# Kernel tuning notes

Hardware: AMD Instinct MI355X
Metric: run time of the kernel (lower is better)

The kernel has to match this reference:

```python
import jax, jax.numpy as jnp
import numpy as np

D_MODEL = 512
NUM_HEADS = 8
HEAD_DIM = D_MODEL // NUM_HEADS
BATCH = 4
SEQ = 2048
NEG_INF = -1e9  # large negative instead of -inf so fully-masked rows stay finite


def setup_inputs() -> dict:
    key = jax.random.key(0)
    k1, k2, k3, k4 = jax.random.split(key, 4)
    x = jax.random.normal(k1, (BATCH, SEQ, D_MODEL), dtype=jnp.float32)
    mask = jnp.zeros((1, 1, SEQ, SEQ), dtype=jnp.float32)  # unused: paded_mask path taken
    paded_mask = jax.random.randint(k2, (BATCH, SEQ), 0, 2).astype(bool)
    W_qkv = jax.random.normal(k3, (D_MODEL, 3 * D_MODEL), dtype=jnp.float32) * (D_MODEL ** -0.5)
    W_out = jax.random.normal(k4, (D_MODEL, D_MODEL), dtype=jnp.float32) * (D_MODEL ** -0.5)
    return {"x": x, "mask": mask, "paded_mask": paded_mask, "W_qkv": W_qkv, "W_out": W_out}


def reference(x, mask, paded_mask, W_qkv, W_out):
    B, S, D = x.shape
    H, hd = NUM_HEADS, HEAD_DIM
    qkv = x @ W_qkv                                   # [B,S,3D]
    # Faithful to original: reshape (NOT transpose) (B,S,H,3hd) -> (B,H,S,3hd)
    qkv = qkv.reshape(B, S, H, 3 * hd).reshape(B, H, S, 3 * hd)
    q, k, v = jnp.split(qkv, 3, axis=3)               # each [B,H,S,hd]
    scaled = jnp.einsum("bhqd,bhkd->bhqk", q, k) / (hd ** 0.5)
    valid = paded_mask.astype(scaled.dtype)           # [B,S]
    # masked_padding_Decoder: softmax over valid keys for valid query rows,
    # zeros on invalid rows and invalid columns.
    logits = jnp.where(paded_mask[:, None, None, :], scaled, NEG_INF)
    att = jax.nn.softmax(logits, axis=-1)
    att = att * valid[:, None, :, None] * valid[:, None, None, :]
    values = jnp.einsum("bhqk,bhkd->bhqd", att, v)    # [B,H,S,hd]
    # Faithful to original: plain reshape (B,H,S,hd) -> (B,S,D)
    values = values.reshape(B, S, H * hd)
    return values @ W_out
```

## Files before the change

kernel.cpp:

```cpp
#include <hip/hip_runtime.h>
#include <hip/hip_bf16.h>
#include <math.h>
#include <stdint.h>

#define BATCH   4
#define SEQ     2048
#define DMODEL  512
#define NHEADS  8
#define HDIM    64
#define QKV_N   (3*DMODEL)

typedef short bf8  __attribute__((ext_vector_type(8)));
typedef float f32x4 __attribute__((ext_vector_type(4)));

#define MFMA16(a,b,c) __builtin_amdgcn_mfma_f32_16x16x32_bf16((a),(b),(c),0,0,0)

__device__ inline unsigned short f2bf(float f){
  unsigned int u = __float_as_uint(f);
  u += 0x7FFFu + ((u >> 16) & 1u);
  return (unsigned short)(u >> 16);
}

__device__ inline unsigned int pack_bf2(float a, float b){
  __hip_bfloat162 h = __float22bfloat162_rn(make_float2(a, b));
  return *reinterpret_cast<unsigned int*>(&h);
}

__device__ __forceinline__ float exp2_hw(float x){
#if defined(__has_builtin)
#if __has_builtin(__builtin_amdgcn_exp2f)
  return __builtin_amdgcn_exp2f(x);
#else
  float r; asm("v_exp_f32 %0, %1" : "=v"(r) : "v"(x)); return r;
#endif
#else
  float r; asm("v_exp_f32 %0, %1" : "=v"(r) : "v"(x)); return r;
#endif
}

__device__ __forceinline__ void gload_lds16(const unsigned short* g,
                                            unsigned short* l){
  __builtin_amdgcn_global_load_lds(
      (const __attribute__((address_space(1))) unsigned int*)g,
      (__attribute__((address_space(3))) unsigned int*)l,
      16, 0, 0);
}

__global__ __launch_bounds__(256) void prep(
    const float* __restrict__ x, const float* __restrict__ Wqkv,
    const float* __restrict__ Wout, unsigned short* __restrict__ Xh,
    unsigned short* __restrict__ WqkvT, unsigned short* __restrict__ WoutT)
{
  __shared__ unsigned short Ts[64][72];
  const int t = threadIdx.x;
  const int bx = blockIdx.x;
  if (bx < 2048) {
    const int i = bx*256 + t;
    const float4 a = reinterpret_cast<const float4*>(x)[2*i];
    const float4 b = reinterpret_cast<const float4*>(x)[2*i+1];
    uint4 o; unsigned short* us = reinterpret_cast<unsigned short*>(&o);
    us[0]=f2bf(a.x); us[1]=f2bf(a.y); us[2]=f2bf(a.z); us[3]=f2bf(a.w);
    us[4]=f2bf(b.x); us[5]=f2bf(b.y); us[6]=f2bf(b.z); us[7]=f2bf(b.w);
    reinterpret_cast<uint4*>(Xh)[i] = o;
    return;
  }
  const float* in; unsigned short* out; int R, C, gx, gy;
  if (bx < 2048 + 192) {
    const int bid = bx - 2048;
    gx = bid % 24; gy = bid / 24; in = Wqkv; out = WqkvT; R = DMODEL; C = QKV_N;
  } else {
    const int bid = bx - 2240;
    gx = bid % 8;  gy = bid / 8;  in = Wout; out = WoutT; R = DMODEL; C = DMODEL;
  }
  const int r0 = gy<<6, c0 = gx<<6;
  const int rr = t>>2, cs = (t&3)<<4;
#pragma unroll
  for (int p=0;p<4;++p){
    float4 v = *reinterpret_cast<const float4*>(in + (size_t)(r0+rr)*C + c0 + cs + p*4);
    Ts[rr][cs+p*4+0]=f2bf(v.x); Ts[rr][cs+p*4+1]=f2bf(v.y);
    Ts[rr][cs+p*4+2]=f2bf(v.z); Ts[rr][cs+p*4+3]=f2bf(v.w);
  }
  __syncthreads();
  const int cc = t>>2, rs = (t&3)<<4;
#pragma unroll
  for (int p=0;p<4;++p){
    ushort4 o;
    o.x = Ts[rs+p*4+0][cc]; o.y = Ts[rs+p*4+1][cc];
    o.z = Ts[rs+p*4+2][cc]; o.w = Ts[rs+p*4+3][cc];
    *reinterpret_cast<ushort4*>(out + (size_t)(c0+cc)*R + r0 + rs + p*4) = o;
  }
}

__global__ __launch_bounds__(256) void gemm_qkv_mfma(
    const unsigned short* __restrict__ A, const unsigned short* __restrict__ Bt,
    unsigned short* __restrict__ QKV)
{
  __shared__ unsigned short As[128][64];
  __shared__ unsigned short Bs[128][64];
  const int t = threadIdx.x;
  const int w = t>>6, lane = t&63, quad = lane>>4, l15 = lane&15;
  const int wr = (w>>1)<<6, wc = (w&1)<<6;
  const int linear = blockIdx.y*12 + blockIdx.x;
  const int swz = (linear & 7)*96 + (linear >> 3);
  const int m0 = (swz/12)<<7, n0 = (swz%12)<<7;
  const int row = t>>3, seg = t&7;
  const unsigned short* Agp = A  + (size_t)(m0+row)*DMODEL + seg*8;
  const unsigned short* Bgp = Bt + (size_t)(n0+row)*DMODEL + seg*8;
  f32x4 acc[4][4];
#pragma unroll
  for (int i=0;i<4;++i)
#pragma unroll
    for (int j=0;j<4;++j) acc[i][j] = (f32x4){0.f,0.f,0.f,0.f};

  for (int k0=0;k0<DMODEL;k0+=64){
    __syncthreads();
#pragma unroll
    for (int p=0;p<4;++p){
      gload_lds16(Agp + (size_t)p*32*DMODEL + k0, &As[(w<<3)+(p<<5)][0]);
      gload_lds16(Bgp + (size_t)p*32*DMODEL + k0, &Bs[(w<<3)+(p<<5)][0]);
    }
    __syncthreads();
#pragma unroll
    for (int ks=0;ks<2;++ks){
      bf8 af[4], bfr[4];
#pragma unroll
      for (int mi=0;mi<4;++mi)
        af[mi]  = *reinterpret_cast<const bf8*>(&As[wr+mi*16+l15][ks*32+quad*8]);
#pragma unroll
      for (int nj=0;nj<4;++nj)
        bfr[nj] = *reinterpret_cast<const bf8*>(&Bs[wc+(l15<<2)+nj][ks*32+quad*8]);
#pragma unroll
      for (int mi=0;mi<4;++mi)
#pragma unroll
        for (int nj=0;nj<4;++nj) acc[mi][nj] = MFMA16(af[mi], bfr[nj], acc[mi][nj]);
    }
  }
  const int cbase = n0 + wc + (l15<<2);
  bool isq[4];
#pragma unroll
  for (int nj=0;nj<4;++nj) isq[nj] = ((cbase+nj) % 192) < 64;
#pragma unroll
  for (int mi=0;mi<4;++mi)
#pragma unroll
    for (int i=0;i<4;++i){
      const int m = m0 + wr + mi*16 + quad*4 + i;
      unsigned long long pk = 0;
#pragma unroll
      for (int nj=0;nj<4;++nj){
        float v = acc[mi][nj][i];
        if (isq[nj]) v *= 0.18033688f;
        pk |= (unsigned long long)f2bf(v) << (16*nj);
      }
      *reinterpret_cast<unsigned long long*>(QKV + (size_t)m*QKV_N + cbase) = pk;
    }
}

__global__ __launch_bounds__(256) void v_transpose(
    const unsigned short* __restrict__ QKV, unsigned short* __restrict__ VT)
{
  __shared__ unsigned short Td[64][76];
  const int t = threadIdx.x;
  const int bh = blockIdx.y, b = bh>>3, hp = bh&7;
  const int s0 = blockIdx.x<<6;
  const size_t rbase = (size_t)(b*SEQ + hp*256);
  const int sr = t>>2, db = (t&3)<<4;
  const int kk = s0 + sr;
  const unsigned short* vp =
      QKV + (rbase + (kk>>3))*QKV_N + (kk&7)*192 + 128 + db;
  uint4 a = *reinterpret_cast<const uint4*>(vp);
  uint4 c = *reinterpret_cast<const uint4*>(vp + 8);
  const unsigned short* ua = reinterpret_cast<const unsigned short*>(&a);
  const unsigned short* uc = reinterpret_cast<const unsigned short*>(&c);
#pragma unroll
  for (int j=0;j<8;++j) Td[db+j][sr]   = ua[j];
#pragma unroll
  for (int j=0;j<8;++j) Td[db+8+j][sr] = uc[j];
  __syncthreads();
  const int L = t&15, d0 = t>>4;
  unsigned short* Op = VT + (size_t)bh*HDIM*SEQ + s0 + (L<<2);
#pragma unroll
  for (int cc=0;cc<4;++cc){
    const int d = d0 + (cc<<4);
    *reinterpret_cast<unsigned long long*>(Op + (size_t)d*SEQ) =
        *reinterpret_cast<const unsigned long long*>(&Td[d][L<<2]);
  }
}

__global__ __launch_bounds__(512, 4) void attn_mfma(
    const unsigned short* __restrict__ QKV, const unsigned short* __restrict__ VT,
    const int* __restrict__ mask, unsigned short* __restrict__ O)
{
  __shared__ unsigned long long mbits[32];
  __shared__ unsigned short Ks[2][64][72];
  __shared__ unsigned short Vs[2][64][72];
  __shared__ unsigned short Pl[8][16][72];
  const int t = threadIdx.x;
  const int w = t>>6, lane = t&63, quad = lane>>4, l15 = lane&15;
  const int linear = blockIdx.y*16 + blockIdx.x;
  const int swz = (linear & 7)*64 + (linear >> 3);
  const int bh = swz >> 4, b = bh>>3, hp = bh&7;
  const int q0 = (swz & 15) << 7;
  const int qs = q0 + (w<<4);
  const int* mb = mask + b*SEQ;
  const f32x4 Z4 = {0.f,0.f,0.f,0.f};
#pragma unroll
  for (int i=0;i<4;++i){
    const unsigned long long bal = __ballot(mb[i*512 + t] != 0);
    if (lane == 0) mbits[i*8 + w] = bal;
  }

  const size_t rbase = (size_t)(b*SEQ + hp*256);
  bf8 qf[2];
  {
    const int q = qs + l15;
    const unsigned short* qp =
        QKV + (rbase + (q>>3))*QKV_N + (q&7)*192 + (quad<<3);
    qf[0] = *reinterpret_cast<const bf8*>(qp);
    qf[1] = *reinterpret_cast<const bf8*>(qp + 32);
  }
  const unsigned short* Vg = VT + (size_t)bh*HDIM*SEQ;

  bf8 ones;
#pragma unroll
  for (int j=0;j<8;++j) ones[j] = (short)0x3F80;

  const int srow = t>>3, sc8 = (t&7)<<3;
  const int krow = ((srow&3)<<4) + (srow>>2);

  f32x4 of[4]; f32x4 lsv = Z4;
#pragma unroll
  for (int i=0;i<4;++i) of[i]=Z4;

  uint4 gk0, gv0;
  {
    const unsigned short* kp =
        QKV + (rbase + (srow>>3))*QKV_N + (srow&7)*192 + 64 + sc8;
    gk0 = *reinterpret_cast<const uint4*>(kp);
    gv0 = *reinterpret_cast<const uint4*>(Vg + (size_t)srow*SEQ + sc8);
  }
  *reinterpret_cast<uint4*>(&Ks[0][krow][sc8]) = gk0;
  *reinterpret_cast<uint4*>(&Vs[0][srow][sc8]) = gv0;
  {
    const int kk = 64 + srow;
    const unsigned short* kp =
        QKV + (rbase + (kk>>3))*QKV_N + (kk&7)*192 + 64 + sc8;
    gk0 = *reinterpret_cast<const uint4*>(kp);
    gv0 = *reinterpret_cast<const uint4*>(Vg + (size_t)srow*SEQ + 64 + sc8);
  }
  __syncthreads();

  auto iter = [&](unsigned short (&KSC)[64][72], unsigned short (&VSC)[64][72],
                  unsigned short (&KSN)[64][72], unsigned short (&VSN)[64][72],
                  int kt) {
    if (kt + 64 < SEQ){
      *reinterpret_cast<uint4*>(&KSN[krow][sc8]) = gk0;
      *reinterpret_cast<uint4*>(&VSN[srow][sc8]) = gv0;
    }
    if (kt + 128 < SEQ){
      const int kk = kt + 128 + srow;
      const unsigned short* kp =
          QKV + (rbase + (kk>>3))*QKV_N + (kk&7)*192 + 64 + sc8;
      gk0 = *reinterpret_cast<const uint4*>(kp);
      gv0 = *reinterpret_cast<const uint4*>(
          Vg + (size_t)srow*SEQ + (kt + 128) + sc8);
    }

    const unsigned int msel =
        (unsigned int)(mbits[kt>>6] >> (l15<<2)) & 0xFu;

    bf8 kf[4][2];
#pragma unroll
    for (int nf=0;nf<4;++nf){
      kf[nf][0] = *reinterpret_cast<const bf8*>(&KSC[nf*16+l15][quad<<3]);
      kf[nf][1] = *reinterpret_cast<const bf8*>(&KSC[nf*16+l15][32+(quad<<3)]);
    }

    f32x4 sc[4];
    __builtin_amdgcn_s_setprio(1);
#pragma unroll
    for (int nf=0;nf<4;++nf){
      f32x4 s = MFMA16(qf[0], kf[nf][0], Z4);
      sc[nf] = MFMA16(qf[1], kf[nf][1], s);
    }
    __builtin_amdgcn_s_setprio(0);
    float pv[4][4];
#pragma unroll
    for (int nf=0;nf<4;++nf){
      const bool on = (msel >> nf) & 1u;
#pragma unroll
      for (int i=0;i<4;++i)
        pv[nf][i] = on ? exp2_hw(sc[nf][i]) : 0.f;
    }
#pragma unroll
    for (int i=0;i<4;++i){
      const unsigned int lo = pack_bf2(pv[0][i], pv[1][i]);
      const unsigned int hi = pack_bf2(pv[2][i], pv[3][i]);
      *reinterpret_cast<unsigned long long*>(&Pl[w][(quad<<2)+i][l15<<2]) =
          ((unsigned long long)hi<<32) | lo;
    }

    bf8 pa[2];
    pa[0] = *reinterpret_cast<const bf8*>(&Pl[w][l15][quad<<3]);
    pa[1] = *reinterpret_cast<const bf8*>(&Pl[w][l15][32+(quad<<3)]);
    __builtin_amdgcn_s_setprio(1);
    {
      f32x4 l = MFMA16(pa[0], ones, lsv);
      lsv = MFMA16(pa[1], ones, l);
    }
#pragma unroll
    for (int nf=0;nf<4;++nf){
      const bf8 v0 = *reinterpret_cast<const bf8*>(&VSC[nf*16+l15][quad<<3]);
      const bf8 v1 = *reinterpret_cast<const bf8*>(&VSC[nf*16+l15][32+(quad<<3)]);
      f32x4 o = MFMA16(pa[0], v0, of[nf]);
      of[nf] = MFMA16(pa[1], v1, o);
    }
    __builtin_amdgcn_s_setprio(0);
    __syncthreads();
  };

  for (int kt=0; kt<SEQ; kt+=128){
    iter(Ks[0], Vs[0], Ks[1], Vs[1], kt);
    iter(Ks[1], Vs[1], Ks[0], Vs[0], kt+64);
  }

  unsigned short* Op = O + (size_t)bh*SEQ*HDIM;
  const unsigned long long qw = mbits[qs >> 6];
#pragma unroll
  for (int i=0;i<4;++i){
    const int q = qs + (quad<<2) + i;
    const bool qv = (qw >> (q & 63)) & 1ull;
    const float l = lsv[i];
    const float inv = (qv && l > 0.f) ? 1.f/l : 0.f;
#pragma unroll
    for (int nf=0;nf<4;++nf)
      Op[(size_t)q*HDIM + (nf<<4) + l15] = f2bf(of[nf][i]*inv);
  }
}

__global__ __launch_bounds__(256) void gemm_out_mfma(
    const unsigned short* __restrict__ A, const unsigned short* __restrict__ Bt,
    float* __restrict__ Out)
{
  __shared__ unsigned short As[128][64];
  __shared__ unsigned short Bs[64][64];
  const int t = threadIdx.x;
  const int w = t>>6, lane = t&63, quad = lane>>4, l15 = lane&15;
  const int wr = (w>>1)<<6, wc = (w&1)<<5;
  const int linear = blockIdx.y*8 + blockIdx.x;
  const int swz = (linear & 7)*64 + (linear >> 3);
  const int m0 = (swz>>3)<<7, n0 = (swz&7)<<6;
  const int row = t>>3, seg = t&7;
  const unsigned short* Agp = A  + (size_t)(m0+row)*DMODEL + seg*8;
  const unsigned short* Bgp = Bt + (size_t)(n0+row)*DMODEL + seg*8;
  f32x4 acc[4][2];
#pragma unroll
  for (int i=0;i<4;++i)
#pragma unroll
    for (int j=0;j<2;++j) acc[i][j] = (f32x4){0.f,0.f,0.f,0.f};

  for (int k0=0;k0<DMODEL;k0+=64){
    __syncthreads();
#pragma unroll
    for (int p=0;p<4;++p)
      gload_lds16(Agp + (size_t)p*32*DMODEL + k0, &As[(w<<3)+(p<<5)][0]);
#pragma unroll
    for (int p=0;p<2;++p)
      gload_lds16(Bgp + (size_t)p*32*DMODEL + k0, &Bs[(w<<3)+(p<<5)][0]);
    __syncthreads();
#pragma unroll
    for (int ks=0;ks<2;++ks){
      bf8 af[4], bfr[2];
#pragma unroll
      for (int mi=0;mi<4;++mi)
        af[mi]  = *reinterpret_cast<const bf8*>(&As[wr+mi*16+l15][ks*32+quad*8]);
#pragma unroll
      for (int nj=0;nj<2;++nj)
        bfr[nj] = *reinterpret_cast<const bf8*>(&Bs[wc+(l15<<1)+nj][ks*32+quad*8]);
#pragma unroll
      for (int mi=0;mi<4;++mi)
#pragma unroll
        for (int nj=0;nj<2;++nj) acc[mi][nj] = MFMA16(af[mi], bfr[nj], acc[mi][nj]);
    }
  }
  const int cbase = n0 + wc + (l15<<1);
#pragma unroll
  for (int mi=0;mi<4;++mi)
#pragma unroll
    for (int i=0;i<4;++i){
      const int m = m0 + wr + mi*16 + quad*4 + i;
      const float2 o = make_float2(acc[mi][0][i], acc[mi][1][i]);
      *reinterpret_cast<float2*>(Out + (size_t)m*DMODEL + cbase) = o;
    }
}

extern "C" void kernel_launch(void* const* d_in, const int* in_sizes, int n_in,
                              void* d_out, int out_size, void* d_ws, size_t ws_size,
                              hipStream_t stream) {
  (void)in_sizes; (void)n_in; (void)out_size; (void)ws_size;
  const float* x     = (const float*)d_in[0];
  const int*   pmask = (const int*)d_in[2];
  const float* Wqkv  = (const float*)d_in[3];
  const float* Wout  = (const float*)d_in[4];
  float* out = (float*)d_out;

  const size_t per = (size_t)BATCH*NHEADS*SEQ*HDIM;
  unsigned short* Xh    = (unsigned short*)d_ws;
  unsigned short* WqkvT = Xh    + (size_t)8192*512;
  unsigned short* WoutT = WqkvT + (size_t)1536*512;
  unsigned short* QKVb  = WoutT + (size_t)512*512;
  unsigned short* VbT   = QKVb  + (size_t)8192*QKV_N;
  unsigned short* Ob    = VbT + per;

  prep<<<2304, 256, 0, stream>>>(x, Wqkv, Wout, Xh, WqkvT, WoutT);
  gemm_qkv_mfma<<<dim3(QKV_N/128, 8192/128), 256, 0, stream>>>(Xh, WqkvT, QKVb);
  v_transpose<<<dim3(SEQ/64, BATCH*NHEADS), 256, 0, stream>>>(QKVb, VbT);
  attn_mfma<<<dim3(SEQ/128, BATCH*NHEADS), 512, 0, stream>>>(QKVb, VbT, pmask, Ob);
  gemm_out_mfma<<<dim3(DMODEL/64, 8192/128), 256, 0, stream>>>(Ob, WoutT, out);
}
```

Measured before the change: 190.3 us.

## Compact valid keys per batch and iterate attention only over them

A new prep pass prefix-sums the padding mask per batch into a compacted index list of valid key positions plus a count. The V transpose and the K loads in attention gather through this index list, and the attention loop stops at the rounded-up valid count. This skips the QK, exp and PV work for padded keys, which is about half of them with the random mask. In exchange, K loads become gathers rather than contiguous reads, and a scan with block barriers is added to prep.

```diff
diff --git a/kernel.cpp b/kernel.cpp
--- a/kernel.cpp
+++ b/kernel.cpp
@@ -48,10 +48,14 @@
 
 __global__ __launch_bounds__(256) void prep(
     const float* __restrict__ x, const float* __restrict__ Wqkv,
-    const float* __restrict__ Wout, unsigned short* __restrict__ Xh,
-    unsigned short* __restrict__ WqkvT, unsigned short* __restrict__ WoutT)
+    const float* __restrict__ Wout, const int* __restrict__ pmask,
+    unsigned short* __restrict__ Xh, unsigned short* __restrict__ WqkvT,
+    unsigned short* __restrict__ WoutT, int* __restrict__ Idx,
+    int* __restrict__ Cnt)
 {
   __shared__ unsigned short Ts[64][72];
+  __shared__ int ps[256];
+  __shared__ int tot;
   const int t = threadIdx.x;
   const int bx = blockIdx.x;
   if (bx < 2048) {
@@ -62,6 +66,25 @@
     us[0]=f2bf(a.x); us[1]=f2bf(a.y); us[2]=f2bf(a.z); us[3]=f2bf(a.w);
     us[4]=f2bf(b.x); us[5]=f2bf(b.y); us[6]=f2bf(b.z); us[7]=f2bf(b.w);
     reinterpret_cast<uint4*>(Xh)[i] = o;
+    return;
+  }
+  if (bx >= 2304) {
+    const int b = bx - 2304;
+    const int* mb = pmask + b*SEQ;
+    int loc[8]; int c = 0; const int base = t*8;
+#pragma unroll
+    for (int j=0;j<8;++j){ const int v = (mb[base+j] != 0); loc[j]=v; c+=v; }
+    ps[t] = c; __syncthreads();
+    for (int off=1; off<256; off<<=1){
+      const int v = (t>=off) ? ps[t-off] : 0;
+      __syncthreads(); ps[t] += v; __syncthreads();
+    }
+    int excl = ps[t] - c;
+#pragma unroll
+    for (int j=0;j<8;++j) if (loc[j]) Idx[b*SEQ + (excl++)] = base + j;
+    if (t == 255){ Cnt[b] = ps[255]; tot = ps[255]; }
+    __syncthreads();
+    for (int k = tot + t; k < SEQ; k += 256) Idx[b*SEQ + k] = 0;
     return;
   }
   const float* in; unsigned short* out; int R, C, gx, gy;
@@ -156,7 +179,8 @@
 }
 
 __global__ __launch_bounds__(256) void v_transpose(
-    const unsigned short* __restrict__ QKV, unsigned short* __restrict__ VT)
+    const unsigned short* __restrict__ QKV, const int* __restrict__ Idx,
+    unsigned short* __restrict__ VT)
 {
   __shared__ unsigned short Td[64][76];
   const int t = threadIdx.x;
@@ -164,9 +188,9 @@
   const int s0 = blockIdx.x<<6;
   const size_t rbase = (size_t)(b*SEQ + hp*256);
   const int sr = t>>2, db = (t&3)<<4;
-  const int kk = s0 + sr;
+  const int s = Idx[b*SEQ + s0 + sr];
   const unsigned short* vp =
-      QKV + (rbase + (kk>>3))*QKV_N + (kk&7)*192 + 128 + db;
+      QKV + (rbase + (s>>3))*QKV_N + (s&7)*192 + 128 + db;
   uint4 a = *reinterpret_cast<const uint4*>(vp);
   uint4 c = *reinterpret_cast<const uint4*>(vp + 8);
   const unsigned short* ua = reinterpret_cast<const unsigned short*>(&a);
@@ -188,7 +212,8 @@
 
 __global__ __launch_bounds__(512, 4) void attn_mfma(
     const unsigned short* __restrict__ QKV, const unsigned short* __restrict__ VT,
-    const int* __restrict__ mask, unsigned short* __restrict__ O)
+    const int* __restrict__ mask, const int* __restrict__ Idx,
+    const int* __restrict__ Cnt, unsigned short* __restrict__ O)
 {
   __shared__ unsigned long long mbits[32];
   __shared__ unsigned short Ks[2][64][72];
@@ -208,6 +233,9 @@
     const unsigned long long bal = __ballot(mb[i*512 + t] != 0);
     if (lane == 0) mbits[i*8 + w] = bal;
   }
+  const int kcnt = Cnt[b];
+  const int kend = ((kcnt + 63) >> 6) << 6;
+  const int* Idxb = Idx + b*SEQ;
 
   const size_t rbase = (size_t)(b*SEQ + hp*256);
   bf8 qf[2];
@@ -233,17 +261,18 @@
 
   uint4 gk0, gv0;
   {
+    const int s = Idxb[srow];
     const unsigned short* kp =
-        QKV + (rbase + (srow>>3))*QKV_N + (srow&7)*192 + 64 + sc8;
+        QKV + (rbase + (s>>3))*QKV_N + (s&7)*192 + 64 + sc8;
     gk0 = *reinterpret_cast<const uint4*>(kp);
     gv0 = *reinterpret_cast<const uint4*>(Vg + (size_t)srow*SEQ + sc8);
   }
   *reinterpret_cast<uint4*>(&Ks[0][krow][sc8]) = gk0;
   *reinterpret_cast<uint4*>(&Vs[0][srow][sc8]) = gv0;
   {
-    const int kk = 64 + srow;
+    const int s = Idxb[64 + srow];
     const unsigned short* kp =
-        QKV + (rbase + (kk>>3))*QKV_N + (kk&7)*192 + 64 + sc8;
+        QKV + (rbase + (s>>3))*QKV_N + (s&7)*192 + 64 + sc8;
     gk0 = *reinterpret_cast<const uint4*>(kp);
     gv0 = *reinterpret_cast<const uint4*>(Vg + (size_t)srow*SEQ + 64 + sc8);
   }
@@ -252,22 +281,19 @@
   auto iter = [&](unsigned short (&KSC)[64][72], unsigned short (&VSC)[64][72],
                   unsigned short (&KSN)[64][72], unsigned short (&VSN)[64][72],
                   int kt) {
-    if (kt + 64 < SEQ){
+    if (kt + 64 < kend){
       *reinterpret_cast<uint4*>(&KSN[krow][sc8]) = gk0;
       *reinterpret_cast<uint4*>(&VSN[srow][sc8]) = gv0;
     }
-    if (kt + 128 < SEQ){
-      const int kk = kt + 128 + srow;
+    if (kt + 128 < kend){
+      const int s = Idxb[kt + 128 + srow];
       const unsigned short* kp =
-          QKV + (rbase + (kk>>3))*QKV_N + (kk&7)*192 + 64 + sc8;
+          QKV + (rbase + (s>>3))*QKV_N + (s&7)*192 + 64 + sc8;
       gk0 = *reinterpret_cast<const uint4*>(kp);
       gv0 = *reinterpret_cast<const uint4*>(
           Vg + (size_t)srow*SEQ + (kt + 128) + sc8);
     }
 
-    const unsigned int msel =
-        (unsigned int)(mbits[kt>>6] >> (l15<<2)) & 0xFu;
-
     bf8 kf[4][2];
 #pragma unroll
     for (int nf=0;nf<4;++nf){
@@ -283,10 +309,11 @@
       sc[nf] = MFMA16(qf[1], kf[nf][1], s);
     }
     __builtin_amdgcn_s_setprio(0);
+    const int kbase = kt + (l15<<2);
     float pv[4][4];
 #pragma unroll
     for (int nf=0;nf<4;++nf){
-      const bool on = (msel >> nf) & 1u;
+      const bool on = (kbase + nf) < kcnt;
 #pragma unroll
       for (int i=0;i<4;++i)
         pv[nf][i] = on ? exp2_hw(sc[nf][i]) : 0.f;
@@ -318,9 +345,10 @@
     __syncthreads();
   };
 
-  for (int kt=0; kt<SEQ; kt+=128){
+  for (int kt=0; kt<kend; kt+=128){
     iter(Ks[0], Vs[0], Ks[1], Vs[1], kt);
-    iter(Ks[1], Vs[1], Ks[0], Vs[0], kt+64);
+    if (kt + 64 < kend)
+      iter(Ks[1], Vs[1], Ks[0], Vs[0], kt+64);
   }
 
   unsigned short* Op = O + (size_t)bh*SEQ*HDIM;
@@ -410,10 +438,14 @@
   unsigned short* QKVb  = WoutT + (size_t)512*512;
   unsigned short* VbT   = QKVb  + (size_t)8192*QKV_N;
   unsigned short* Ob    = VbT + per;
-
-  prep<<<2304, 256, 0, stream>>>(x, Wqkv, Wout, Xh, WqkvT, WoutT);
+  int* Idx = (int*)(Ob + per);
+  int* Cnt = Idx + (size_t)BATCH*SEQ;
+
+  prep<<<2308, 256, 0, stream>>>(x, Wqkv, Wout, pmask, Xh, WqkvT, WoutT,
+                                 Idx, Cnt);
   gemm_qkv_mfma<<<dim3(QKV_N/128, 8192/128), 256, 0, stream>>>(Xh, WqkvT, QKVb);
-  v_transpose<<<dim3(SEQ/64, BATCH*NHEADS), 256, 0, stream>>>(QKVb, VbT);
-  attn_mfma<<<dim3(SEQ/128, BATCH*NHEADS), 512, 0, stream>>>(QKVb, VbT, pmask, Ob);
+  v_transpose<<<dim3(SEQ/64, BATCH*NHEADS), 256, 0, stream>>>(QKVb, Idx, VbT);
+  attn_mfma<<<dim3(SEQ/128, BATCH*NHEADS), 512, 0, stream>>>(
+      QKVb, VbT, pmask, Idx, Cnt, Ob);
   gemm_out_mfma<<<dim3(DMODEL/64, 8192/128), 256, 0, stream>>>(Ob, WoutT, out);
 }
```

Result: faster. 170.8 us (-10.2%).
